# Kernel optimization log

Measured on AMD Instinct MI355X. Metric: run time of the kernel, lower is better.

The kernel has to match this reference:

```python
import jax, jax.numpy as jnp
import numpy as np

H = 4            # attention heads
D_SUB = 32       # per-head hidden dim
D_HID = H * D_SUB
B = 100          # graphs in batch
N_PER = 5000     # nodes per graph
N = B * N_PER
DEG = 16         # avg degree
E = N * DEG
K_PER = 2500     # ceil(0.5 * N_PER), pooling_rate=0.5


def setup_inputs() -> dict:
    key = jax.random.key(0)
    k0, k1, k2, k3 = jax.random.split(key, 4)
    x = jax.random.normal(k0, (N, D_HID), jnp.float32)
    sub_xs = jax.random.normal(k1, (H, N, D_SUB), jnp.float32)
    # edges strictly within each graph (contiguous node blocks per graph)
    rng = np.random.default_rng(0)
    src = rng.integers(0, N_PER, size=(B, N_PER * DEG))
    dst = rng.integers(0, N_PER, size=(B, N_PER * DEG))
    off = (np.arange(B) * N_PER)[:, None]
    edge_index = jnp.asarray(
        np.stack([(src + off).reshape(-1), (dst + off).reshape(-1)]), jnp.int32)
    batch = jnp.repeat(jnp.arange(B, dtype=jnp.int32), N_PER)
    att_W = jax.random.normal(k2, (H, D_SUB, 1), jnp.float32) * 0.1
    att_b = jnp.zeros((H, 1), jnp.float32)
    score_W = jax.random.normal(k3, (1, 1), jnp.float32)
    score_b = jnp.zeros((1,), jnp.float32)
    return {"x": x, "sub_xs": sub_xs, "att_W": att_W, "att_b": att_b,
            "score_W": score_W, "score_b": score_b,
            "edge_index": edge_index, "batch": batch}


def _gcn_prop(h, row, col, dis):
    # PyG GCNConv propagation with self-loops: D^{-1/2}(A+I)D^{-1/2} h
    norm = (dis[row] * dis[col])[:, None]                       # [E,1]
    agg = jax.ops.segment_sum(h[row] * norm, col, num_segments=N)
    return agg + h * (dis ** 2)[:, None]                        # self-loop term deg^-1


def reference(x, sub_xs, att_W, att_b, score_W, score_b, edge_index, batch):
    row, col = edge_index[0], edge_index[1]
    deg = 1.0 + jax.ops.segment_sum(jnp.ones((E,), x.dtype), col, num_segments=N)
    dis = deg ** -0.5
    # per-head GCNConv(sub_hidden, 1): [H,N,1]
    h = jnp.einsum('hnd,hdo->hno', sub_xs, att_W)
    agg = jax.vmap(lambda hh: _gcn_prop(hh, row, col, dis))(h) + att_b[:, None, :]
    # torch F.softmax with implicit dim=1 on [N,1] -> softmax over size-1 axis (all ones); faithful
    att = jax.nn.softmax(agg, axis=-1)                          # [H,N,1]
    pool = att.mean(axis=0)                                     # 'mean' att pooling -> [N,1]
    # pooling_score_layer = GCNConv(1,1)
    score = (_gcn_prop(pool @ score_W, row, col, dis) + score_b)[:, 0]  # [N]
    # batched topk: equal-size contiguous graphs -> static k per graph
    _, idx = jax.lax.top_k(score.reshape(B, N_PER), K_PER)      # sorted desc per graph
    perm = (idx + (jnp.arange(B) * N_PER)[:, None]).reshape(-1) # [B*K_PER]
    x_new = x[perm] * jnp.tanh(score[perm])[:, None]            # global att weighting
    batch_new = batch[perm]
    # filter_adj: keep edges with both endpoints selected, reindex to new ids
    n_idx = jnp.full((N,), -1, jnp.int32).at[perm].set(
        jnp.arange(B * K_PER, dtype=jnp.int32))
    r, c = n_idx[row], n_idx[col]
    keep = (r >= 0) & (c >= 0)
    pos = jnp.nonzero(keep, size=E, fill_value=0)[0]            # compacted, order-preserving
    valid = jnp.arange(E) < keep.sum()
    edge_new = jnp.stack([jnp.where(valid, r[pos], -1),
                          jnp.where(valid, c[pos], -1)])        # [2,E], -1 padded
    return x_new, edge_new, batch_new, perm
```

## Files before the change

### kernel.cpp

```cpp
#include <hip/hip_runtime.h>
#include <hip/hip_bf16.h>

constexpr int H      = 4;
constexpr int D_SUB  = 32;
constexpr int D_HID  = 128;
constexpr int B      = 100;
constexpr int N_PER  = 5000;
constexpr int N      = B * N_PER;
constexpr int DEG    = 16;
constexpr int E      = N * DEG;
constexpr int E_PER  = N_PER * DEG;
constexpr int K_PER  = 2500;
constexpr int NK     = B * K_PER;

constexpr int EPB    = 4096;
constexpr int EPT    = 16;
constexpr int NBLK_E = (E + EPB - 1) / EPB;

constexpr int SUBR   = 625;
constexpr int LCAP   = 11640;
constexpr int NEPOCH = 8;
constexpr int EP_I4  = (E_PER / 4) / NEPOCH;

constexpr int M      = 8192;

constexpr unsigned long long FLG_A = 1ull << 62;
constexpr unsigned long long FLG_I = 2ull << 62;

__device__ __forceinline__ int swz8(int bid, int chunk) {
    return (bid & 7) * chunk + (bid >> 3);
}

__device__ __forceinline__ int ph(int i) { return i + (i >> 3); }

__global__ __launch_bounds__(1024) void k_count(const int* __restrict__ col,
                                                int* __restrict__ cnt2) {
    __shared__ int h[N_PER];
    int lb = swz8(blockIdx.x, 25);
    int g = lb >> 1, half = lb & 1;
    for (int i = threadIdx.x; i < N_PER; i += 1024) h[i] = 0;
    __syncthreads();
    int ebase = g * E_PER + half * (E_PER / 2);
    int nbase = g * N_PER;
    const int4* c4 = (const int4*)(col + ebase);
    for (int i = threadIdx.x; i < E_PER / 2 / 4; i += 1024) {
        int4 v = c4[i];
        atomicAdd(&h[v.x - nbase], 1);
        atomicAdd(&h[v.y - nbase], 1);
        atomicAdd(&h[v.z - nbase], 1);
        atomicAdd(&h[v.w - nbase], 1);
    }
    __syncthreads();
    int* dst = cnt2 + half * N + nbase;
    for (int i = threadIdx.x; i < N_PER; i += 1024) dst[i] = h[i];
}

__global__ void k_dis(const int4* __restrict__ cnt2a, const int4* __restrict__ cnt2b,
                      int4* __restrict__ cnt, float4* __restrict__ dis) {
    int i = blockIdx.x * blockDim.x + threadIdx.x;
    if (i < N / 4) {
        int4 a = cnt2a[i], b = cnt2b[i];
        int4 c = make_int4(a.x + b.x, a.y + b.y, a.z + b.z, a.w + b.w);
        cnt[i] = c;
        float4 d;
        d.x = __fdiv_rn(1.0f, __fsqrt_rn((float)(1 + c.x)));
        d.y = __fdiv_rn(1.0f, __fsqrt_rn((float)(1 + c.y)));
        d.z = __fdiv_rn(1.0f, __fsqrt_rn((float)(1 + c.z)));
        d.w = __fdiv_rn(1.0f, __fsqrt_rn((float)(1 + c.w)));
        dis[i] = d;
    }
}

__global__ __launch_bounds__(1024) void k_score_fused(const int* __restrict__ row,
                                                      const int* __restrict__ col,
                                                      const int* __restrict__ cnt,
                                                      const float* __restrict__ dis,
                                                      const float* __restrict__ scW,
                                                      const float* __restrict__ scB,
                                                      float* __restrict__ score) {
    __shared__ float dis_l[N_PER];
    __shared__ int   wsum[16];
    __shared__ int   offs_l[SUBR];
    __shared__ int   curs_l[SUBR];
    __shared__ int   list[LCAP];
    int lb = swz8(blockIdx.x, 100);
    int g = lb >> 3, q = lb & 7;
    int t = threadIdx.x;
    int nbase = g * N_PER;
    int ebase = g * E_PER;
    int lo = q * SUBR;

    const float4* d4 = (const float4*)(dis + nbase);
    for (int j4 = t; j4 < N_PER / 4; j4 += 1024) {
        float4 dv4 = d4[j4];
        int j = 4 * j4;
        dis_l[j]     = dv4.x;
        dis_l[j + 1] = dv4.y;
        dis_l[j + 2] = dv4.z;
        dis_l[j + 3] = dv4.w;
    }

    int v = (t < SUBR) ? cnt[nbase + lo + t] : 0;
    int lane = t & 63, wid = t >> 6;
    int x = v;
#pragma unroll
    for (int s = 1; s < 64; s <<= 1) {
        int o = __shfl_up(x, s, 64);
        if (lane >= s) x += o;
    }
    if (lane == 63) wsum[wid] = x;
    __syncthreads();
    if (wid == 0) {
        int ws = (lane < 16) ? wsum[lane] : 0;
#pragma unroll
        for (int s = 1; s < 16; s <<= 1) {
            int o = __shfl_up(ws, s, 64);
            if (lane >= s) ws += o;
        }
        if (lane < 16) wsum[lane] = ws;
    }
    __syncthreads();
    int incl = x + (wid > 0 ? wsum[wid - 1] : 0);
    if (t < SUBR) { offs_l[t] = incl - v + t; curs_l[t] = 0; }
    __syncthreads();

    const int4* c4 = (const int4*)(col + ebase);
    const int4* r4 = (const int4*)(row + ebase);
    for (int ep = 0; ep < NEPOCH; ep++) {
        for (int i4 = ep * EP_I4 + t; i4 < (ep + 1) * EP_I4; i4 += 1024) {
            int4 cv = c4[i4];
            int4 rv = r4[i4];
            int i0 = 4 * i4;
#pragma unroll
            for (int m = 0; m < 4; m++) {
                int cl = ((m == 0) ? cv.x : (m == 1) ? cv.y : (m == 2) ? cv.z : cv.w) - nbase;
                int rl = ((m == 0) ? rv.x : (m == 1) ? rv.y : (m == 2) ? rv.z : rv.w) - nbase;
                unsigned d = (unsigned)(cl - lo);
                if (d < (unsigned)SUBR) {
                    int i = i0 + m;
                    int slot = atomicAdd(&curs_l[d], 1);
                    int pos = offs_l[d] + slot;
                    if (pos < LCAP) list[pos] = (i << 13) | rl;
                }
            }
        }
        __syncthreads();
    }

    if (t < SUBR) {
        int base = offs_l[t];
        int k = v;
        if (base + k > LCAP) k = 0;
        for (int i = 1; i < k; i++) {
            int key = list[base + i];
            int j = i - 1;
            while (j >= 0 && list[base + j] > key) { list[base + j + 1] = list[base + j]; j--; }
            list[base + j + 1] = key;
        }
        float w = scW[0];
        float dv = dis_l[lo + t];
        float s = 0.0f;
        for (int i = 0; i < k; i++) {
            int rl = list[base + i] & 8191;
            s = __fadd_rn(s, __fmul_rn(w, __fmul_rn(dis_l[rl], dv)));
        }
        s = __fadd_rn(s, __fmul_rn(w, __fmul_rn(dv, dv)));
        s = __fadd_rn(s, scB[0]);
        score[nbase + lo + t] = s;
    }
}

__global__ __launch_bounds__(1024) void k_topk(const float* __restrict__ score,
                                               float* __restrict__ out_batch,
                                               float* __restrict__ out_perm,
                                               int* __restrict__ perm_i,
                                               int* __restrict__ n_idx) {
    __shared__ unsigned long long keys[M + (M >> 3)];
    int b = blockIdx.x, t = threadIdx.x;
    int base = 8 * t;

    unsigned long long v[8];
    if (t < 625) {
        const float4* s4 = (const float4*)(score + b * N_PER + base);
        float4 f0 = s4[0], f1 = s4[1];
        float fs[8] = {f0.x, f0.y, f0.z, f0.w, f1.x, f1.y, f1.z, f1.w};
#pragma unroll
        for (int m = 0; m < 8; m++) {
            unsigned u = __float_as_uint(fs[m]);
            unsigned asc = u ^ ((u & 0x80000000u) ? 0xFFFFFFFFu : 0x80000000u);
            v[m] = ((unsigned long long)(~asc) << 32) | (unsigned)(base + m);
        }
    } else {
#pragma unroll
        for (int m = 0; m < 8; m++) v[m] = ~0ull;
    }

#define CEV(x, y, up) { if ((v[x] > v[y]) == (up)) { unsigned long long tmp = v[x]; v[x] = v[y]; v[y] = tmp; } }
    CEV(0, 1, true)  CEV(2, 3, false) CEV(4, 5, true)  CEV(6, 7, false)
    CEV(0, 2, true)  CEV(1, 3, true)  CEV(4, 6, false) CEV(5, 7, false)
    CEV(0, 1, true)  CEV(2, 3, true)  CEV(4, 5, false) CEV(6, 7, false)
    {
        bool u8 = ((t & 1) == 0);
        CEV(0, 4, u8) CEV(1, 5, u8) CEV(2, 6, u8) CEV(3, 7, u8)
        CEV(0, 2, u8) CEV(1, 3, u8) CEV(4, 6, u8) CEV(5, 7, u8)
        CEV(0, 1, u8) CEV(2, 3, u8) CEV(4, 5, u8) CEV(6, 7, u8)
    }
#pragma unroll
    for (int m = 0; m < 8; m++) keys[ph(base + m)] = v[m];
    __syncthreads();

    for (int k = 16; k <= M; k <<= 1) {
        bool last = (k == M);
        for (int j = k >> 1; j >= 8; j >>= 1) {
            int np = (last && j < (M >> 1)) ? (M >> 2) : (M >> 1);
            for (int p = t; p < np; p += 1024) {
                int i = ((p & ~(j - 1)) << 1) | (p & (j - 1));
                int ip = i | j;
                bool up = ((i & k) == 0);
                unsigned long long a = keys[ph(i)];
                unsigned long long c = keys[ph(ip)];
                if ((a > c) == up) { keys[ph(i)] = c; keys[ph(ip)] = a; }
            }
            __syncthreads();
        }
        int nb = last ? 512 : 1024;
        if (t < nb) {
            bool up = ((base & k) == 0);
            unsigned long long w[8];
#pragma unroll
            for (int m = 0; m < 8; m++) w[m] = keys[ph(base + m)];
#define CEW(x, y) { if ((w[x] > w[y]) == up) { unsigned long long tmp = w[x]; w[x] = w[y]; w[y] = tmp; } }
            CEW(0, 4) CEW(1, 5) CEW(2, 6) CEW(3, 7)
            CEW(0, 2) CEW(1, 3) CEW(4, 6) CEW(5, 7)
            CEW(0, 1) CEW(2, 3) CEW(4, 5) CEW(6, 7)
#pragma unroll
            for (int m = 0; m < 8; m++) keys[ph(base + m)] = w[m];
        }
        __syncthreads();
    }

    for (int r = t; r < K_PER; r += 1024) {
        unsigned long long key = keys[ph(r)];
        int idx = (int)(key & 0xFFFFFFFFull);
        int gl = b * N_PER + idx;
        int ni = b * K_PER + r;
        perm_i[ni] = gl;
        n_idx[gl] = ni;
        out_perm[ni] = (float)gl;
        out_batch[ni] = (float)b;
    }
}

__global__ void k_xnew(const float4* __restrict__ x4, const float* __restrict__ score,
                       const int* __restrict__ perm_i, float4* __restrict__ out4) {
    int tid = blockIdx.x * blockDim.x + threadIdx.x;
    if (tid >= NK * (D_HID / 4)) return;
    int i = tid >> 5;
    int c = tid & 31;
    int g = perm_i[i];
    float ts = tanhf(score[g]);
    float4 v = x4[(long)g * 32 + c];
    v.x *= ts; v.y *= ts; v.z *= ts; v.w *= ts;
    out4[tid] = v;
}

__global__ void k_prefill(float4* __restrict__ oe0, float4* __restrict__ oe1,
                          int4* __restrict__ n_idx4,
                          unsigned long long* __restrict__ status) {
    int i = blockIdx.x * blockDim.x + threadIdx.x;
    int stride = gridDim.x * blockDim.x;
    float4 m1 = make_float4(-1.0f, -1.0f, -1.0f, -1.0f);
    for (int j = i; j < E / 4; j += stride) { oe0[j] = m1; oe1[j] = m1; }
    int4 mi = make_int4(-1, -1, -1, -1);
    for (int j = i; j < N / 4; j += stride) n_idx4[j] = mi;
    for (int j = i; j < NBLK_E; j += stride) status[j] = 0ull;
}

__global__ __launch_bounds__(256) void k_compact(const int* __restrict__ row,
                                                 const int* __restrict__ col,
                                                 const int* __restrict__ n_idx,
                                                 unsigned long long* __restrict__ status,
                                                 float* __restrict__ oe0,
                                                 float* __restrict__ oe1) {
    __shared__ int wsum[4];
    __shared__ int excl_sh;
    int blk = blockIdx.x, t = threadIdx.x;
    int base = blk * EPB + t * EPT;
    int rr[EPT], cc[EPT];
    int cnt = 0;
    if (blk < NBLK_E - 1) {
#pragma unroll
        for (int i4 = 0; i4 < 4; i4++) {
            int4 rv = ((const int4*)(row + base))[i4];
            int4 cv = ((const int4*)(col + base))[i4];
            rr[4 * i4 + 0] = n_idx[rv.x];  cc[4 * i4 + 0] = n_idx[cv.x];
            rr[4 * i4 + 1] = n_idx[rv.y];  cc[4 * i4 + 1] = n_idx[cv.y];
            rr[4 * i4 + 2] = n_idx[rv.z];  cc[4 * i4 + 2] = n_idx[cv.z];
            rr[4 * i4 + 3] = n_idx[rv.w];  cc[4 * i4 + 3] = n_idx[cv.w];
        }
#pragma unroll
        for (int i = 0; i < EPT; i++)
            if (rr[i] >= 0 && cc[i] >= 0) cnt++;
    } else {
#pragma unroll
        for (int i = 0; i < EPT; i++) {
            int e = base + i;
            int rv = -1, cv = -1;
            if (e < E) { rv = n_idx[row[e]]; cv = n_idx[col[e]]; }
            rr[i] = rv; cc[i] = cv;
            if (rv >= 0 && cv >= 0) cnt++;
        }
    }
    int lane = t & 63, wid = t >> 6;
    int x = cnt;
#pragma unroll
    for (int s = 1; s < 64; s <<= 1) {
        int o = __shfl_up(x, s, 64);
        if (lane >= s) x += o;
    }
    if (lane == 63) wsum[wid] = x;
    __syncthreads();
    if (t == 0) {
        int a0 = wsum[0], a1 = wsum[1], a2 = wsum[2];
        wsum[1] = a0; wsum[2] = a0 + a1; wsum[3] = a0 + a1 + a2;
        wsum[0] = 0;
    }
    __syncthreads();
    int incl = x + wsum[wid];
    int agg;
    {
        __shared__ int agg_sh;
        if (t == 255) agg_sh = incl;
        __syncthreads();
        agg = agg_sh;
    }
    if (t == 0) {
        if (blk == 0) {
            atomicExch(&status[0], FLG_I | (unsigned long long)(unsigned)agg);
            excl_sh = 0;
        } else {
            atomicExch(&status[blk], FLG_A | (unsigned long long)(unsigned)agg);
            unsigned long long ex = 0;
            for (int i = blk - 1; i >= 0; i--) {
                unsigned long long sv;
                do { sv = atomicAdd(&status[i], 0ull); } while (sv == 0ull);
                ex += (sv & 0xFFFFFFFFull);
                if (sv & FLG_I) break;
            }
            atomicExch(&status[blk], FLG_I | (ex + (unsigned long long)(unsigned)agg));
            excl_sh = (int)ex;
        }
    }
    __syncthreads();
    int pos = excl_sh + incl - cnt;
#pragma unroll
    for (int i = 0; i < EPT; i++) {
        if (rr[i] >= 0 && cc[i] >= 0) {
            oe0[pos] = (float)rr[i];
            oe1[pos] = (float)cc[i];
            pos++;
        }
    }
}

extern "C" void kernel_launch(void* const* d_in, const int* in_sizes, int n_in,
                              void* d_out, int out_size, void* d_ws, size_t ws_size,
                              hipStream_t stream) {
    const float* x   = (const float*)d_in[0];
    const float* scW = (const float*)d_in[4];
    const float* scB = (const float*)d_in[5];
    const int*   edge = (const int*)d_in[6];
    const int*   row = edge;
    const int*   col = edge + E;

    unsigned long long* status = (unsigned long long*)d_ws;
    int*   ws_i    = (int*)(status + NBLK_E);
    int*   cnt2    = ws_i;
    int*   deg_cnt = ws_i + 2 * N;
    float* dis     = (float*)(ws_i + 3 * N);
    float* score   = (float*)(ws_i + 4 * N);
    int*   n_idx   = ws_i + 5 * N;
    int*   perm_i  = ws_i + 6 * N;

    float* out_x     = (float*)d_out;
    float* oe0       = out_x + (size_t)NK * D_HID;
    float* oe1       = oe0 + E;
    float* out_batch = oe1 + E;
    float* out_perm  = out_batch + NK;

    k_prefill<<<2048, 256, 0, stream>>>((float4*)oe0, (float4*)oe1, (int4*)n_idx, status);
    k_count<<<200, 1024, 0, stream>>>(col, cnt2);
    k_dis<<<(N / 4 + 255) / 256, 256, 0, stream>>>((const int4*)cnt2, (const int4*)(cnt2 + N),
                                                   (int4*)deg_cnt, (float4*)dis);
    k_score_fused<<<800, 1024, 0, stream>>>(row, col, deg_cnt, dis, scW, scB, score);
    k_topk<<<B, 1024, 0, stream>>>(score, out_batch, out_perm, perm_i, n_idx);
    k_xnew<<<(NK * (D_HID / 4) + 255) / 256, 256, 0, stream>>>((const float4*)x, score, perm_i,
                                                               (float4*)out_x);
    k_compact<<<NBLK_E, 256, 0, stream>>>(row, col, n_idx, status, oe0, oe1);
}
```

Measured before the change: 256.1 us.

## Fill only the edge-output tail and halve score kernel blocks per graph

The full -1 prefill of both edge output arrays is removed. A new kernel reads the compacted edge count from the last decoupled-lookback status entry and writes -1 only after that point, so kept slots are no longer written twice. The fused score kernel now splits each graph into 4 node subranges of 1250 instead of 8 of 625, which means each block rescans the graph's edge list fewer times, at the cost of larger shared memory per block and fewer blocks. The scan now handles two nodes per thread, and the sort loop reads counts from the cursors.

Measured after the change: 269.0 us. 5.0% more time.

```diff
diff --git a/kernel.cpp b/kernel.cpp
--- a/kernel.cpp
+++ b/kernel.cpp
@@ -17,8 +17,8 @@
 constexpr int EPT    = 16;
 constexpr int NBLK_E = (E + EPB - 1) / EPB;
 
-constexpr int SUBR   = 625;
-constexpr int LCAP   = 11640;
+constexpr int SUBR   = 1250;
+constexpr int LCAP   = 22250;
 constexpr int NEPOCH = 8;
 constexpr int EP_I4  = (E_PER / 4) / NEPOCH;
 
@@ -83,8 +83,8 @@
     __shared__ int   offs_l[SUBR];
     __shared__ int   curs_l[SUBR];
     __shared__ int   list[LCAP];
-    int lb = swz8(blockIdx.x, 100);
-    int g = lb >> 3, q = lb & 7;
+    int lb = swz8(blockIdx.x, 50);
+    int g = lb >> 2, q = lb & 3;
     int t = threadIdx.x;
     int nbase = g * N_PER;
     int ebase = g * E_PER;
@@ -100,9 +100,14 @@
         dis_l[j + 3] = dv4.w;
     }
 
-    int v = (t < SUBR) ? cnt[nbase + lo + t] : 0;
+    int va = 0, vb = 0;
+    if (t < SUBR / 2) {
+        va = cnt[nbase + lo + 2 * t];
+        vb = cnt[nbase + lo + 2 * t + 1];
+    }
+    int pair = va + vb;
     int lane = t & 63, wid = t >> 6;
-    int x = v;
+    int x = pair;
 #pragma unroll
     for (int s = 1; s < 64; s <<= 1) {
         int o = __shfl_up(x, s, 64);
@@ -120,8 +125,14 @@
         if (lane < 16) wsum[lane] = ws;
     }
     __syncthreads();
-    int incl = x + (wid > 0 ? wsum[wid - 1] : 0);
-    if (t < SUBR) { offs_l[t] = incl - v + t; curs_l[t] = 0; }
+    if (t < SUBR / 2) {
+        int incl = x + (wid > 0 ? wsum[wid - 1] : 0);
+        int excl = incl - pair;
+        offs_l[2 * t]     = excl + 2 * t;
+        offs_l[2 * t + 1] = excl + va + 2 * t + 1;
+        curs_l[2 * t] = 0;
+        curs_l[2 * t + 1] = 0;
+    }
     __syncthreads();
 
     const int4* c4 = (const int4*)(col + ebase);
@@ -147,9 +158,11 @@
         __syncthreads();
     }
 
-    if (t < SUBR) {
-        int base = offs_l[t];
-        int k = v;
+    float w  = scW[0];
+    float sb = scB[0];
+    for (int n = t; n < SUBR; n += 1024) {
+        int base = offs_l[n];
+        int k = curs_l[n];
         if (base + k > LCAP) k = 0;
         for (int i = 1; i < k; i++) {
             int key = list[base + i];
@@ -157,16 +170,15 @@
             while (j >= 0 && list[base + j] > key) { list[base + j + 1] = list[base + j]; j--; }
             list[base + j + 1] = key;
         }
-        float w = scW[0];
-        float dv = dis_l[lo + t];
+        float dv = dis_l[lo + n];
         float s = 0.0f;
         for (int i = 0; i < k; i++) {
             int rl = list[base + i] & 8191;
             s = __fadd_rn(s, __fmul_rn(w, __fmul_rn(dis_l[rl], dv)));
         }
         s = __fadd_rn(s, __fmul_rn(w, __fmul_rn(dv, dv)));
-        s = __fadd_rn(s, scB[0]);
-        score[nbase + lo + t] = s;
+        s = __fadd_rn(s, sb);
+        score[nbase + lo + n] = s;
     }
 }
 
@@ -264,13 +276,10 @@
     out4[tid] = v;
 }
 
-__global__ void k_prefill(float4* __restrict__ oe0, float4* __restrict__ oe1,
-                          int4* __restrict__ n_idx4,
+__global__ void k_prefill(int4* __restrict__ n_idx4,
                           unsigned long long* __restrict__ status) {
     int i = blockIdx.x * blockDim.x + threadIdx.x;
     int stride = gridDim.x * blockDim.x;
-    float4 m1 = make_float4(-1.0f, -1.0f, -1.0f, -1.0f);
-    for (int j = i; j < E / 4; j += stride) { oe0[j] = m1; oe1[j] = m1; }
     int4 mi = make_int4(-1, -1, -1, -1);
     for (int j = i; j < N / 4; j += stride) n_idx4[j] = mi;
     for (int j = i; j < NBLK_E; j += stride) status[j] = 0ull;
@@ -363,6 +372,14 @@
     }
 }
 
+__global__ void k_filltail(const unsigned long long* __restrict__ status,
+                           float* __restrict__ oe0, float* __restrict__ oe1) {
+    int cnt = (int)(status[NBLK_E - 1] & 0xFFFFFFFFull);
+    int i = blockIdx.x * blockDim.x + threadIdx.x;
+    int stride = gridDim.x * blockDim.x;
+    for (int j = cnt + i; j < E; j += stride) { oe0[j] = -1.0f; oe1[j] = -1.0f; }
+}
+
 extern "C" void kernel_launch(void* const* d_in, const int* in_sizes, int n_in,
                               void* d_out, int out_size, void* d_ws, size_t ws_size,
                               hipStream_t stream) {
@@ -388,13 +405,14 @@
     float* out_batch = oe1 + E;
     float* out_perm  = out_batch + NK;
 
-    k_prefill<<<2048, 256, 0, stream>>>((float4*)oe0, (float4*)oe1, (int4*)n_idx, status);
+    k_prefill<<<1024, 256, 0, stream>>>((int4*)n_idx, status);
     k_count<<<200, 1024, 0, stream>>>(col, cnt2);
     k_dis<<<(N / 4 + 255) / 256, 256, 0, stream>>>((const int4*)cnt2, (const int4*)(cnt2 + N),
                                                    (int4*)deg_cnt, (float4*)dis);
-    k_score_fused<<<800, 1024, 0, stream>>>(row, col, deg_cnt, dis, scW, scB, score);
+    k_score_fused<<<400, 1024, 0, stream>>>(row, col, deg_cnt, dis, scW, scB, score);
     k_topk<<<B, 1024, 0, stream>>>(score, out_batch, out_perm, perm_i, n_idx);
     k_xnew<<<(NK * (D_HID / 4) + 255) / 256, 256, 0, stream>>>((const float4*)x, score, perm_i,
                                                                (float4*)out_x);
     k_compact<<<NBLK_E, 256, 0, stream>>>(row, col, n_idx, status, oe0, oe1);
-}
+    k_filltail<<<4096, 256, 0, stream>>>(status, oe0, oe1);
+}
```
